# Performance work log

Measured on AMD Instinct MI355X. Metric: run time of the kernel, lower is better.

## Reference

```python
import jax, jax.numpy as jnp
import numpy as np

DIM, HEADS = 1536, 12
HD = DIM // HEADS            # 128 head dim
C = HD // 2                  # 64 complex (pair) dim
C0 = C - 2 * (C // 3)        # 22 (temporal axis)
C1 = C // 3                  # 21 (each spatial axis)
MAX_POS = 1024
F_, H_, W_ = 9, 22, 22
SEQ = F_ * H_ * W_           # 4356
NCLASS = 2
EPS = 1e-6


def _rope_tables():
    # Wan rope_params: theta = 10000, per-axis half-dims C0, C1, C1.
    def ang(half):
        inv = 1.0 / (10000.0 ** (np.arange(0, 2 * half, 2) / (2 * half)))
        return np.outer(np.arange(MAX_POS), inv)
    a = np.concatenate([ang(C0), ang(C1), ang(C1)], axis=1)  # [MAX_POS, C]
    return jnp.asarray(np.cos(a), jnp.float32), jnp.asarray(np.sin(a), jnp.float32)


def setup_inputs() -> dict:
    key = jax.random.key(0)
    ks = jax.random.split(key, 6)
    s = 1.0 / np.sqrt(DIM)
    def lin(k):
        k1, k2 = jax.random.split(k)
        return (jax.random.uniform(k1, (DIM, DIM), jnp.float32, -s, s),
                jax.random.uniform(k2, (DIM,), jnp.float32, -s, s))
    Wq, bq = lin(ks[0]); Wk, bk = lin(ks[1]); Wv, bv = lin(ks[2]); Wo, bo = lin(ks[3])
    fc, fs = _rope_tables()
    masks = (jax.random.uniform(ks[4], (NCLASS, H_ * W_)) < 0.5).astype(jnp.float32)
    x = jax.random.normal(ks[5], (1, SEQ, DIM), jnp.float32)
    return {"x": x, "Wq": Wq, "bq": bq, "Wk": Wk, "bk": bk, "Wv": Wv, "bv": bv,
            "Wo": Wo, "bo": bo, "gq": jnp.ones((DIM,), jnp.float32),
            "gk": jnp.ones((DIM,), jnp.float32), "freqs_cos": fc, "freqs_sin": fs,
            "ref_target_masks": masks, "f": F_, "h": H_, "w": W_}


def _rmsnorm(x, g):
    return x * jax.lax.rsqrt(jnp.mean(x * x, axis=-1, keepdims=True) + EPS) * g


def _grid_cs(tab, f, h, w):
    # per-position (f,h,w) rope table -> [f*h*w, C]
    p0 = jnp.broadcast_to(tab[:f, None, None, :C0], (f, h, w, C0))
    p1 = jnp.broadcast_to(tab[None, :h, None, C0:C0 + C1], (f, h, w, C1))
    p2 = jnp.broadcast_to(tab[None, None, :w, C0 + C1:], (f, h, w, C1))
    return jnp.concatenate([p0, p1, p2], axis=-1).reshape(f * h * w, C)


def _rope(x, cos, sin):
    # x: [b,s,n,d]; pairs are interleaved along d (view_as_complex semantics)
    b, s, n, d = x.shape
    xr = x.reshape(b, s, n, d // 2, 2)
    a, bi = xr[..., 0], xr[..., 1]
    cos = cos[None, :, None, :]
    sin = sin[None, :, None, :]
    out = jnp.stack([a * cos - bi * sin, a * sin + bi * cos], axis=-1)
    return out.reshape(b, s, n, d)


def reference(x, Wq, bq, Wk, bk, Wv, bv, Wo, bo, gq, gk, freqs_cos, freqs_sin,
              ref_target_masks, f, h, w):
    b, s, _ = x.shape
    n, d = HEADS, HD
    q = _rmsnorm(x @ Wq.T + bq, gq).reshape(b, s, n, d)
    k = _rmsnorm(x @ Wk.T + bk, gk).reshape(b, s, n, d)
    v = (x @ Wv.T + bv).reshape(b, s, n, d)
    cos = _grid_cs(freqs_cos, f, h, w)
    sin = _grid_cs(freqs_sin, f, h, w)
    q = _rope(q, cos, sin)
    k = _rope(k, cos, sin)
    scale = 1.0 / np.sqrt(d).astype(np.float32)
    # full (window_size == (-1,-1)) attention; seq_lens == s so k_lens mask is identity
    scores = jnp.einsum('bsnd,btnd->bnst', q, k) * scale
    p = jax.nn.softmax(scores, axis=-1)
    o = jnp.einsum('bnst,btnd->bsnd', p, v).reshape(b, s, n * d)
    out = o @ Wo.T + bo
    # aux attention map vs reference-frame keys (first h*w spatial tokens), no-grad path
    xs = h * w
    ref_k = k[:, :xs]
    s2 = jnp.einsum('bsnd,btnd->bnst', q * scale, ref_k)
    p2 = jax.nn.softmax(s2, axis=-1)                       # [b,n,s,xs]
    m = ref_target_masks                                   # [c,xs]
    maps = jnp.einsum('bnst,ct->cbns', p2, m) / jnp.sum(m, axis=-1)[:, None, None, None]
    attn_map = maps.mean(axis=2).reshape(-1, s)            # mean over heads -> [c*b, s]
    return out, attn_map
```

## Files before the change

kernel.cpp:

```cpp
#include <hip/hip_runtime.h>
#include <hip/hip_bf16.h>
#include <math.h>

constexpr int SEQ   = 4356;
constexpr int DIM   = 1536;
constexpr int HEADS = 12;
constexpr int HD    = 128;
constexpr int CH    = 64;
constexpr int C0c   = 22;
constexpr int C1c   = 21;
constexpr int WWc   = 22;
constexpr int HHWW  = 484;
constexpr int XS    = 484;
constexpr int KVB   = 32;
constexpr int NT    = (SEQ + KVB - 1) / KVB;
constexpr int SEQP  = 4416;
constexpr size_t SD = (size_t)SEQ * DIM;

typedef float f32x4 __attribute__((ext_vector_type(4)));
typedef short bf16x8 __attribute__((ext_vector_type(8)));
typedef short bf16x4 __attribute__((ext_vector_type(4)));

__device__ inline unsigned short f2bf(float f) {
  union { float f; unsigned u; } x; x.f = f;
  return (unsigned short)((x.u + 0x7FFFu + ((x.u >> 16) & 1u)) >> 16);
}

#define GLD16(g, l)                                                                        \
  __builtin_amdgcn_global_load_lds((const __attribute__((address_space(1))) unsigned*)    \
                                       (const void*)(g),                                  \
                                   (__attribute__((address_space(3))) unsigned*)(void*)(l),\
                                   16, 0, 0)

__global__ __launch_bounds__(256) void prep_kernel(const float* __restrict__ mask,
                                                   float* __restrict__ amap,
                                                   float* __restrict__ cnt,
                                                   float4* __restrict__ msk4) {
  int t = threadIdx.x;
  for (int i = t; i < 2 * SEQ; i += 256) amap[i] = 0.f;
  for (int i = t; i < 512; i += 256) {
    float4 v;
    v.x = (i < XS) ? mask[i] : 0.f;
    v.y = (i < XS) ? mask[XS + i] : 0.f;
    v.z = (i < XS) ? 1.f : 0.f;
    v.w = 0.f;
    msk4[i] = v;
  }
  float c0 = 0.f, c1 = 0.f;
  for (int i = t; i < XS; i += 256) { c0 += mask[i]; c1 += mask[XS + i]; }
  __shared__ float red0[256];
  __shared__ float red1[256];
  red0[t] = c0; red1[t] = c1;
  __syncthreads();
  for (int off = 128; off > 0; off >>= 1) {
    if (t < off) { red0[t] += red0[t + off]; red1[t] += red1[t + off]; }
    __syncthreads();
  }
  if (t == 0) { cnt[0] = red0[0]; cnt[1] = red1[0]; }
}

__global__ __launch_bounds__(256) void padzero(unsigned short* __restrict__ vt) {
  const int pad = SEQP - SEQ;
  const int total = DIM * pad;
  for (int i = blockIdx.x * 256 + threadIdx.x; i < total; i += gridDim.x * 256) {
    const int d = i / pad, c = i - d * pad;
    vt[(size_t)d * SEQP + SEQ + c] = 0;
  }
}

__global__ __launch_bounds__(256) void to_bf16(const float* __restrict__ in,
                                               unsigned short* __restrict__ out, int n4) {
  for (int i = blockIdx.x * 256 + threadIdx.x; i < n4; i += gridDim.x * 256) {
    const float4 v = ((const float4*)in)[i];
    ushort4 o;
    o.x = f2bf(v.x); o.y = f2bf(v.y); o.z = f2bf(v.z); o.w = f2bf(v.w);
    ((ushort4*)out)[i] = o;
  }
}

__global__ __launch_bounds__(256) void to_bf16_w(const float* __restrict__ W0, const float* __restrict__ W1,
                                                 const float* __restrict__ W2, const float* __restrict__ W3,
                                                 unsigned short* __restrict__ o0, unsigned short* __restrict__ o1,
                                                 unsigned short* __restrict__ o2, unsigned short* __restrict__ o3,
                                                 int n4) {
  const int z = blockIdx.z;
  const float* in = (z == 0) ? W0 : (z == 1) ? W1 : (z == 2) ? W2 : W3;
  unsigned short* out = (z == 0) ? o0 : (z == 1) ? o1 : (z == 2) ? o2 : o3;
  for (int i = blockIdx.x * 256 + threadIdx.x; i < n4; i += gridDim.x * 256) {
    const float4 v = ((const float4*)in)[i];
    ushort4 o;
    o.x = f2bf(v.x); o.y = f2bf(v.y); o.z = f2bf(v.z); o.w = f2bf(v.w);
    ((ushort4*)out)[i] = o;
  }
}

__global__ __launch_bounds__(256) void gemm_qkv(const unsigned short* __restrict__ A,
                                                const unsigned short* __restrict__ B0,
                                                const unsigned short* __restrict__ B1,
                                                const unsigned short* __restrict__ B2,
                                                const float* __restrict__ bq,
                                                const float* __restrict__ bk,
                                                const float* __restrict__ bv,
                                                float* __restrict__ o0,
                                                float* __restrict__ o1,
                                                unsigned short* __restrict__ vtout,
                                                int M) {
  __shared__ unsigned short As[128 * 64];
  __shared__ unsigned short Bs[128 * 64];
  const int z = blockIdx.z;
  const unsigned short* B = (z == 0) ? B0 : (z == 1) ? B1 : B2;
  const float* bias = (z == 0) ? bq : (z == 1) ? bk : bv;
  const int t    = threadIdx.x;
  const int lane = t & 63;
  const int w    = t >> 6;
  const int wr   = w >> 1, wc = w & 1;
  const int bm = blockIdx.x * 128, bn = blockIdx.y * 128;
  const int lq = lane & 15, lg = lane >> 4;
  f32x4 acc[4][4] = {};
  for (int k0 = 0; k0 < DIM; k0 += 64) {
#pragma unroll
    for (int i = 0; i < 4; ++i) {
      const int idx = i * 256 + t;
      const int row = idx >> 3;
      const int c8  = (idx & 7) * 8;
      const int ga  = min(bm + row, M - 1);
      GLD16(A + (size_t)ga * DIM + k0 + c8, As + idx * 8);
      const int gb  = bn + row;
      GLD16(B + (size_t)gb * DIM + k0 + c8, Bs + idx * 8);
    }
    __syncthreads();
#pragma unroll
    for (int kk = 0; kk < 2; ++kk) {
      bf16x8 af[4], bf[4];
#pragma unroll
      for (int m = 0; m < 4; ++m)
        af[m] = *(const bf16x8*)(As + (wr * 64 + m * 16 + lq) * 64 + kk * 32 + lg * 8);
#pragma unroll
      for (int n = 0; n < 4; ++n)
        bf[n] = *(const bf16x8*)(Bs + (wc * 64 + n * 16 + lq) * 64 + kk * 32 + lg * 8);
#pragma unroll
      for (int m = 0; m < 4; ++m)
#pragma unroll
        for (int n = 0; n < 4; ++n)
          acc[m][n] = __builtin_amdgcn_mfma_f32_16x16x32_bf16(af[m], bf[n], acc[m][n], 0, 0, 0);
    }
    __syncthreads();
  }
#pragma unroll
  for (int n = 0; n < 4; ++n) {
    const int col = bn + wc * 64 + n * 16 + lq;
    const float bv2 = bias[col];
#pragma unroll
    for (int m = 0; m < 4; ++m) {
      const int rm = bm + wr * 64 + m * 16 + lg * 4;
      if (z < 2) {
        float* C = (z == 0) ? o0 : o1;
#pragma unroll
        for (int r = 0; r < 4; ++r) {
          const int row = rm + r;
          if (row < M) C[(size_t)row * DIM + col] = acc[m][n][r] + bv2;
        }
      } else {
        if (rm < M) {
          bf16x4 o;
#pragma unroll
          for (int r = 0; r < 4; ++r) o[r] = (short)f2bf(acc[m][n][r] + bv2);
          *(bf16x4*)(vtout + (size_t)col * SEQP + rm) = o;
        }
      }
    }
  }
}

__global__ __launch_bounds__(256) void gemm_mfma(const unsigned short* __restrict__ A,
                                                 const unsigned short* __restrict__ B,
                                                 const float* __restrict__ bias,
                                                 float* __restrict__ C, int M) {
  __shared__ unsigned short As[128 * 64];
  __shared__ unsigned short Bs[128 * 64];
  const int t    = threadIdx.x;
  const int lane = t & 63;
  const int w    = t >> 6;
  const int wr   = w >> 1, wc = w & 1;
  const int bm = blockIdx.x * 128, bn = blockIdx.y * 128;
  const int lq = lane & 15, lg = lane >> 4;
  f32x4 acc[4][4] = {};
  for (int k0 = 0; k0 < DIM; k0 += 64) {
#pragma unroll
    for (int i = 0; i < 4; ++i) {
      const int idx = i * 256 + t;
      const int row = idx >> 3;
      const int c8  = (idx & 7) * 8;
      const int ga  = min(bm + row, M - 1);
      GLD16(A + (size_t)ga * DIM + k0 + c8, As + idx * 8);
      const int gb  = bn + row;
      GLD16(B + (size_t)gb * DIM + k0 + c8, Bs + idx * 8);
    }
    __syncthreads();
#pragma unroll
    for (int kk = 0; kk < 2; ++kk) {
      bf16x8 af[4], bf[4];
#pragma unroll
      for (int m = 0; m < 4; ++m)
        af[m] = *(const bf16x8*)(As + (wr * 64 + m * 16 + lq) * 64 + kk * 32 + lg * 8);
#pragma unroll
      for (int n = 0; n < 4; ++n)
        bf[n] = *(const bf16x8*)(Bs + (wc * 64 + n * 16 + lq) * 64 + kk * 32 + lg * 8);
#pragma unroll
      for (int m = 0; m < 4; ++m)
#pragma unroll
        for (int n = 0; n < 4; ++n)
          acc[m][n] = __builtin_amdgcn_mfma_f32_16x16x32_bf16(af[m], bf[n], acc[m][n], 0, 0, 0);
    }
    __syncthreads();
  }
#pragma unroll
  for (int n = 0; n < 4; ++n) {
    const int col = bn + wc * 64 + n * 16 + lq;
    const float bv = bias[col];
#pragma unroll
    for (int m = 0; m < 4; ++m) {
      const int rm = bm + wr * 64 + m * 16 + lg * 4;
#pragma unroll
      for (int r = 0; r < 4; ++r) {
        const int row = rm + r;
        if (row < M) C[(size_t)row * DIM + col] = acc[m][n][r] + bv;
      }
    }
  }
}

__global__ __launch_bounds__(256) void rms_rope2(const float* __restrict__ qy,
                                                 const float* __restrict__ ky,
                                                 const float* __restrict__ gq,
                                                 const float* __restrict__ gk,
                                                 const float* __restrict__ fcos,
                                                 const float* __restrict__ fsin,
                                                 unsigned short* __restrict__ qout,
                                                 unsigned short* __restrict__ kout) {
  const int z = blockIdx.y;
  const float* y = z ? ky : qy;
  const float* g = z ? gk : gq;
  unsigned short* outb = z ? kout : qout;
  const float scale = z ? 1.0f : 0.08838834764831845f;
  const int s = blockIdx.x;
  const float* row = y + (size_t)s * DIM;
  const int t = threadIdx.x;
  float ss = 0.f;
  for (int i = t; i < DIM / 4; i += 256) {
    const float4 v = ((const float4*)row)[i];
    ss += v.x * v.x + v.y * v.y + v.z * v.z + v.w * v.w;
  }
#pragma unroll
  for (int off = 1; off < 64; off <<= 1) ss += __shfl_xor(ss, off);
  __shared__ float wred[4];
  if ((t & 63) == 0) wred[t >> 6] = ss;
  __syncthreads();
  const float tot = wred[0] + wred[1] + wred[2] + wred[3];
  const float rs = rsqrtf(tot * (1.0f / DIM) + 1e-6f);
  const int fi  = s / HHWW;
  const int rem = s - fi * HHWW;
  const int hi  = rem / WWc;
  const int wi  = rem - hi * WWc;
  for (int p = t; p < DIM / 2; p += 256) {
    const int head = p >> 6;
    const int c    = p & 63;
    const int idx  = head * HD + 2 * c;
    const int trow = (c < C0c) ? fi : ((c < C0c + C1c) ? hi : wi);
    const float co = fcos[trow * CH + c];
    const float si = fsin[trow * CH + c];
    const float a  = row[idx] * rs * g[idx];
    const float b  = row[idx + 1] * rs * g[idx + 1];
    ushort2 pr;
    pr.x = f2bf((a * co - b * si) * scale);
    pr.y = f2bf((a * si + b * co) * scale);
    *(ushort2*)(outb + (size_t)s * DIM + idx) = pr;
  }
}

#define SOFT_QS(QS, SACC, MAP_, LAST_, KBV)                                                \
  {                                                                                        \
    float sv[8];                                                                           \
    _Pragma("unroll")                                                                      \
    for (int i = 0; i < 8; ++i) {                                                          \
      float v = SACC[i >> 2][i & 3];                                                       \
      if (LAST_) { const int key = (KBV) + (i >> 2) * 16 + lg * 4 + (i & 3);               \
                   if (key >= SEQ) v = -1e30f; }                                           \
      sv[i] = __expf(v);                                                                   \
      ls[QS] += sv[i];                                                                     \
    }                                                                                      \
    if (MAP_) {                                                                            \
      _Pragma("unroll")                                                                    \
      for (int i = 0; i < 8; ++i) {                                                        \
        const int key = (KBV) + (i >> 2) * 16 + lg * 4 + (i & 3);                          \
        const float4 mv = Msk[key];                                                        \
        n0[QS] = fmaf(sv[i], mv.x, n0[QS]);                                                \
        n1[QS] = fmaf(sv[i], mv.y, n1[QS]);                                                \
        d2[QS] = fmaf(sv[i], mv.z, d2[QS]);                                                \
      }                                                                                    \
    }                                                                                      \
    _Pragma("unroll")                                                                      \
    for (int kbi = 0; kbi < 2; ++kbi) {                                                    \
      unsigned r0, r1;                                                                     \
      asm("v_cvt_pk_bf16_f32 %0, %1, %2" : "=v"(r0) : "v"(sv[kbi*4+0]), "v"(sv[kbi*4+1])); \
      asm("v_cvt_pk_bf16_f32 %0, %1, %2" : "=v"(r1) : "v"(sv[kbi*4+2]), "v"(sv[kbi*4+3])); \
      uint2 pw; pw.x = r0; pw.y = r1;                                                      \
      *(uint2*)&Pw[QS][lq][kbi * 16 + lg * 4] = pw;                                        \
    }                                                                                      \
  }

#define TILE_BODY(KB_, MAP_, LAST_, PRE_)                                                  \
  {                                                                                        \
    const int kb_ = (KB_);                                                                 \
    const int cur_ = (kb_ >> 5) & 1;                                                       \
    const unsigned short* Kc = Ks[cur_];                                                   \
    const unsigned short* Vc = Vs[cur_];                                                   \
    if (PRE_) {                                                                            \
      unsigned short* Kn = Ks[cur_ ^ 1];                                                   \
      unsigned short* Vn = Vs[cur_ ^ 1];                                                   \
      const int kbn = kb_ + KVB;                                                           \
      _Pragma("unroll")                                                                    \
      for (int j = 0; j < 2; ++j) {                                                        \
        const int ck = t + j * 256;                                                        \
        const int kr = ck >> 4, ksl = ck & 15;                                             \
        GLD16(kh + (size_t)min(kbn + kr, SEQ - 1) * DIM + ((ksl ^ (kr & 7)) * 8),          \
              Kn + ck * 8);                                                                \
        const int vd = ck >> 2, vsl = ck & 3;                                              \
        GLD16(vh + (size_t)vd * SEQP + kbn + ((vsl ^ ((vd >> 1) & 3)) * 8),                \
              Vn + ck * 8);                                                                \
      }                                                                                    \
    }                                                                                      \
    f32x4 sacc0[2] = {}, sacc1[2] = {};                                                    \
    _Pragma("unroll")                                                                      \
    for (int kbi = 0; kbi < 2; ++kbi) {                                                    \
      const int krow = kbi * 16 + lq;                                                      \
      _Pragma("unroll")                                                                    \
      for (int c = 0; c < 4; ++c) {                                                        \
        const bf16x8 kf = *(const bf16x8*)(Kc + (krow * 16 + ((c * 4 + lg) ^ (krow & 7))) * 8); \
        sacc0[kbi] = __builtin_amdgcn_mfma_f32_16x16x32_bf16(kf, qf0[c], sacc0[kbi], 0, 0, 0);  \
        sacc1[kbi] = __builtin_amdgcn_mfma_f32_16x16x32_bf16(kf, qf1[c], sacc1[kbi], 0, 0, 0);  \
      }                                                                                    \
    }                                                                                      \
    SOFT_QS(0, sacc0, MAP_, LAST_, kb_)                                                    \
    SOFT_QS(1, sacc1, MAP_, LAST_, kb_)                                                    \
    {                                                                                      \
      const bf16x8 pf0 = *(const bf16x8*)&Pw[0][lq][lg * 8];                               \
      const bf16x8 pf1 = *(const bf16x8*)&Pw[1][lq][lg * 8];                               \
      _Pragma("unroll")                                                                    \
      for (int db = 0; db < 8; ++db) {                                                     \
        const int vd = db * 16 + lq;                                                       \
        const bf16x8 vf = *(const bf16x8*)(Vc + (vd * 4 + (lg ^ ((vd >> 1) & 3))) * 8);    \
        acc0[db] = __builtin_amdgcn_mfma_f32_16x16x32_bf16(vf, pf0, acc0[db], 0, 0, 0);    \
        acc1[db] = __builtin_amdgcn_mfma_f32_16x16x32_bf16(vf, pf1, acc1[db], 0, 0, 0);    \
      }                                                                                    \
    }                                                                                      \
    if (PRE_) __syncthreads();                                                             \
  }

__global__ __launch_bounds__(256, 3) void flash_mfma(const unsigned short* __restrict__ qbuf,
                                                     const unsigned short* __restrict__ kbuf,
                                                     const unsigned short* __restrict__ vt,
                                                     const float4* __restrict__ msk4,
                                                     const float* __restrict__ cnt,
                                                     unsigned short* __restrict__ ob,
                                                     float* __restrict__ amap) {
  const int h    = blockIdx.y;
  const int t    = threadIdx.x;
  const int w    = t >> 6;
  const int lane = t & 63;
  const int lq   = lane & 15, lg = lane >> 4;
  const int qbase = blockIdx.x * 128 + w * 32;

  __shared__ __align__(16) unsigned short Ks[2][KVB * 128];
  __shared__ __align__(16) unsigned short Vs[2][128 * KVB];
  __shared__ __align__(16) unsigned short Plds[4][2][16][40];
  __shared__ float4 Msk[512];
  unsigned short (*Pw)[16][40] = Plds[w];

  const unsigned short* kh = kbuf + h * HD;
  const unsigned short* vh = vt + (size_t)(h * HD) * SEQP;

  for (int i = t; i < 512; i += 256) Msk[i] = msk4[i];

  const int qsrc0 = min(qbase + lq, SEQ - 1);
  const int qsrc1 = min(qbase + 16 + lq, SEQ - 1);
  bf16x8 qf0[4], qf1[4];
#pragma unroll
  for (int c = 0; c < 4; ++c) {
    qf0[c] = *(const bf16x8*)(qbuf + (size_t)qsrc0 * DIM + h * HD + c * 32 + lg * 8);
    qf1[c] = *(const bf16x8*)(qbuf + (size_t)qsrc1 * DIM + h * HD + c * 32 + lg * 8);
  }

  f32x4 acc0[8] = {}, acc1[8] = {};
  float ls[2] = {0.f, 0.f};
  float d2[2] = {0.f, 0.f}, n0[2] = {0.f, 0.f}, n1[2] = {0.f, 0.f};

#pragma unroll
  for (int j = 0; j < 2; ++j) {
    const int ck = t + j * 256;
    const int kr = ck >> 4, ksl = ck & 15;
    GLD16(kh + (size_t)min(kr, SEQ - 1) * DIM + ((ksl ^ (kr & 7)) * 8), Ks[0] + ck * 8);
    const int vd = ck >> 2, vsl = ck & 3;
    GLD16(vh + (size_t)vd * SEQP + ((vsl ^ ((vd >> 1) & 3)) * 8), Vs[0] + ck * 8);
  }
  __syncthreads();

  for (int tile = 0; tile < 16; ++tile)         TILE_BODY(tile * KVB, true,  false, true);
  for (int tile = 16; tile < NT - 1; ++tile)    TILE_BODY(tile * KVB, false, false, true);
  TILE_BODY((NT - 1) * KVB, false, true, false);

#pragma unroll
  for (int qs = 0; qs < 2; ++qs) {
    ls[qs] += __shfl_xor(ls[qs], 16);
    ls[qs] += __shfl_xor(ls[qs], 32);
  }
  {
    const int qrow = qbase + lq;
    if (qrow < SEQ) {
      const float inv = 1.f / ls[0];
#pragma unroll
      for (int db = 0; db < 8; ++db) {
        bf16x4 o;
#pragma unroll
        for (int r = 0; r < 4; ++r) o[r] = (short)f2bf(acc0[db][r] * inv);
        *(bf16x4*)(ob + (size_t)qrow * DIM + h * HD + db * 16 + lg * 4) = o;
      }
    }
  }
  {
    const int qrow = qbase + 16 + lq;
    if (qrow < SEQ) {
      const float inv = 1.f / ls[1];
#pragma unroll
      for (int db = 0; db < 8; ++db) {
        bf16x4 o;
#pragma unroll
        for (int r = 0; r < 4; ++r) o[r] = (short)f2bf(acc1[db][r] * inv);
        *(bf16x4*)(ob + (size_t)qrow * DIM + h * HD + db * 16 + lg * 4) = o;
      }
    }
  }
#pragma unroll
  for (int qs = 0; qs < 2; ++qs) {
    float dd = d2[qs], a0 = n0[qs], a1 = n1[qs];
    dd += __shfl_xor(dd, 16); dd += __shfl_xor(dd, 32);
    a0 += __shfl_xor(a0, 16); a0 += __shfl_xor(a0, 32);
    a1 += __shfl_xor(a1, 16); a1 += __shfl_xor(a1, 32);
    const int qrow = qbase + qs * 16 + lq;
    if (lane < 16 && qrow < SEQ) {
      const float invd = 1.f / (dd * (float)HEADS);
      atomicAdd(&amap[qrow],       a0 * invd / cnt[0]);
      atomicAdd(&amap[SEQ + qrow], a1 * invd / cnt[1]);
    }
  }
}

extern "C" void kernel_launch(void* const* d_in, const int* in_sizes, int n_in,
                              void* d_out, int out_size, void* d_ws, size_t ws_size,
                              hipStream_t stream) {
  const float* x    = (const float*)d_in[0];
  const float* Wq   = (const float*)d_in[1];
  const float* bq   = (const float*)d_in[2];
  const float* Wk   = (const float*)d_in[3];
  const float* bk   = (const float*)d_in[4];
  const float* Wv   = (const float*)d_in[5];
  const float* bv   = (const float*)d_in[6];
  const float* Wo   = (const float*)d_in[7];
  const float* bo   = (const float*)d_in[8];
  const float* gq   = (const float*)d_in[9];
  const float* gk   = (const float*)d_in[10];
  const float* fc   = (const float*)d_in[11];
  const float* fs   = (const float*)d_in[12];
  const float* mask = (const float*)d_in[13];

  float* out  = (float*)d_out;
  float* amap = out + SD;
  float* f32a = out;

  float* f32b        = (float*)d_ws;
  unsigned short* xb = (unsigned short*)(f32b + SD);
  unsigned short* qb = xb + SD;
  unsigned short* kb = qb + SD;
  unsigned short* vt = kb + SD;
  unsigned short* wqb = vt + (size_t)DIM * SEQP;
  unsigned short* wkb = wqb + (size_t)DIM * DIM;
  unsigned short* wvb = wkb + (size_t)DIM * DIM;
  unsigned short* wob = wvb + (size_t)DIM * DIM;
  float4* msk4 = (float4*)(wob + (size_t)DIM * DIM);
  float* cnt  = (float*)(msk4 + 512);
  unsigned short* ob = (unsigned short*)f32b;

  prep_kernel<<<1, 256, 0, stream>>>(mask, amap, cnt, msk4);
  padzero<<<64, 256, 0, stream>>>(vt);
  to_bf16<<<2048, 256, 0, stream>>>(x, xb, (int)(SD / 4));
  constexpr int W4 = DIM * DIM / 4;
  to_bf16_w<<<dim3(512, 1, 4), 256, 0, stream>>>(Wq, Wk, Wv, Wo, wqb, wkb, wvb, wob, W4);

  const dim3 gg((SEQ + 127) / 128, DIM / 128, 3);
  gemm_qkv<<<gg, 256, 0, stream>>>(xb, wqb, wkb, wvb, bq, bk, bv, f32a, f32b, vt, SEQ);

  rms_rope2<<<dim3(SEQ, 2), 256, 0, stream>>>(f32a, f32b, gq, gk, fc, fs, qb, kb);

  const dim3 fg((SEQ + 127) / 128, HEADS);
  flash_mfma<<<fg, 256, 0, stream>>>(qb, kb, vt, msk4, cnt, ob, amap);

  const dim3 go((SEQ + 127) / 128, DIM / 128);
  gemm_mfma<<<go, 256, 0, stream>>>(ob, wob, bo, out, SEQ);
}
```

Baseline: 434.1 us.

## Split flash attention across two KV halves and merge with a combine kernel

Adds a second grid dimension so each query block's KV range is processed by two workgroups: the first takes tiles 0–63, including the reference-frame aux map, and the second takes the rest. Each writes unnormalised fp32 accumulators and row sums to scratch buffers. A new combine kernel adds the partials, normalises them and writes the bf16 attention output. The goal is to fill more CUs than the original 420-block grid. The cost is an extra launch plus a large fp32 partial write and read.

```diff
diff --git a/kernel.cpp b/kernel.cpp
--- a/kernel.cpp
+++ b/kernel.cpp
@@ -14,7 +14,9 @@
 constexpr int XS    = 484;
 constexpr int KVB   = 32;
 constexpr int NT    = (SEQ + KVB - 1) / KVB;
+constexpr int TSPLIT = 64;
 constexpr int SEQP  = 4416;
+constexpr int NHQ   = HEADS * SEQ;
 constexpr size_t SD = (size_t)SEQ * DIM;
 
 typedef float f32x4 __attribute__((ext_vector_type(4)));
@@ -362,9 +364,12 @@
                                                      const unsigned short* __restrict__ vt,
                                                      const float4* __restrict__ msk4,
                                                      const float* __restrict__ cnt,
-                                                     unsigned short* __restrict__ ob,
+                                                     float* __restrict__ pacc0,
+                                                     float* __restrict__ pacc1,
+                                                     float* __restrict__ pl,
                                                      float* __restrict__ amap) {
   const int h    = blockIdx.y;
+  const int z    = blockIdx.z;
   const int t    = threadIdx.x;
   const int w    = t >> 6;
   const int lane = t & 63;
@@ -395,63 +400,92 @@
   float ls[2] = {0.f, 0.f};
   float d2[2] = {0.f, 0.f}, n0[2] = {0.f, 0.f}, n1[2] = {0.f, 0.f};
 
+  const int tile0 = (z == 0) ? 0 : TSPLIT;
+  const int kb0   = tile0 * KVB;
+  unsigned short* K0 = Ks[tile0 & 1];
+  unsigned short* V0 = Vs[tile0 & 1];
 #pragma unroll
   for (int j = 0; j < 2; ++j) {
     const int ck = t + j * 256;
     const int kr = ck >> 4, ksl = ck & 15;
-    GLD16(kh + (size_t)min(kr, SEQ - 1) * DIM + ((ksl ^ (kr & 7)) * 8), Ks[0] + ck * 8);
+    GLD16(kh + (size_t)min(kb0 + kr, SEQ - 1) * DIM + ((ksl ^ (kr & 7)) * 8), K0 + ck * 8);
     const int vd = ck >> 2, vsl = ck & 3;
-    GLD16(vh + (size_t)vd * SEQP + ((vsl ^ ((vd >> 1) & 3)) * 8), Vs[0] + ck * 8);
+    GLD16(vh + (size_t)vd * SEQP + kb0 + ((vsl ^ ((vd >> 1) & 3)) * 8), V0 + ck * 8);
   }
   __syncthreads();
 
-  for (int tile = 0; tile < 16; ++tile)         TILE_BODY(tile * KVB, true,  false, true);
-  for (int tile = 16; tile < NT - 1; ++tile)    TILE_BODY(tile * KVB, false, false, true);
-  TILE_BODY((NT - 1) * KVB, false, true, false);
+  if (z == 0) {
+    for (int tile = 0; tile < 16; ++tile)           TILE_BODY(tile * KVB, true,  false, true);
+    for (int tile = 16; tile < TSPLIT - 1; ++tile)  TILE_BODY(tile * KVB, false, false, true);
+    TILE_BODY((TSPLIT - 1) * KVB, false, false, false);
+  } else {
+    for (int tile = TSPLIT; tile < NT - 1; ++tile)  TILE_BODY(tile * KVB, false, false, true);
+    TILE_BODY((NT - 1) * KVB, false, true, false);
+  }
 
 #pragma unroll
   for (int qs = 0; qs < 2; ++qs) {
     ls[qs] += __shfl_xor(ls[qs], 16);
     ls[qs] += __shfl_xor(ls[qs], 32);
   }
+  float* pz  = (z == 0) ? pacc0 : pacc1;
+  float* plz = pl + z * NHQ;
   {
     const int qrow = qbase + lq;
     if (qrow < SEQ) {
-      const float inv = 1.f / ls[0];
-#pragma unroll
-      for (int db = 0; db < 8; ++db) {
-        bf16x4 o;
-#pragma unroll
-        for (int r = 0; r < 4; ++r) o[r] = (short)f2bf(acc0[db][r] * inv);
-        *(bf16x4*)(ob + (size_t)qrow * DIM + h * HD + db * 16 + lg * 4) = o;
-      }
+      float* base = pz + ((size_t)(h * SEQ + qrow)) * HD;
+#pragma unroll
+      for (int db = 0; db < 8; ++db)
+        *(f32x4*)(base + db * 16 + lg * 4) = acc0[db];
+      if (lane < 16) plz[h * SEQ + qrow] = ls[0];
     }
   }
   {
     const int qrow = qbase + 16 + lq;
     if (qrow < SEQ) {
-      const float inv = 1.f / ls[1];
-#pragma unroll
-      for (int db = 0; db < 8; ++db) {
-        bf16x4 o;
-#pragma unroll
-        for (int r = 0; r < 4; ++r) o[r] = (short)f2bf(acc1[db][r] * inv);
-        *(bf16x4*)(ob + (size_t)qrow * DIM + h * HD + db * 16 + lg * 4) = o;
+      float* base = pz + ((size_t)(h * SEQ + qrow)) * HD;
+#pragma unroll
+      for (int db = 0; db < 8; ++db)
+        *(f32x4*)(base + db * 16 + lg * 4) = acc1[db];
+      if (lane < 16) plz[h * SEQ + qrow] = ls[1];
+    }
+  }
+  if (z == 0) {
+#pragma unroll
+    for (int qs = 0; qs < 2; ++qs) {
+      float dd = d2[qs], a0 = n0[qs], a1 = n1[qs];
+      dd += __shfl_xor(dd, 16); dd += __shfl_xor(dd, 32);
+      a0 += __shfl_xor(a0, 16); a0 += __shfl_xor(a0, 32);
+      a1 += __shfl_xor(a1, 16); a1 += __shfl_xor(a1, 32);
+      const int qrow = qbase + qs * 16 + lq;
+      if (lane < 16 && qrow < SEQ) {
+        const float invd = 1.f / (dd * (float)HEADS);
+        atomicAdd(&amap[qrow],       a0 * invd / cnt[0]);
+        atomicAdd(&amap[SEQ + qrow], a1 * invd / cnt[1]);
       }
     }
   }
-#pragma unroll
-  for (int qs = 0; qs < 2; ++qs) {
-    float dd = d2[qs], a0 = n0[qs], a1 = n1[qs];
-    dd += __shfl_xor(dd, 16); dd += __shfl_xor(dd, 32);
-    a0 += __shfl_xor(a0, 16); a0 += __shfl_xor(a0, 32);
-    a1 += __shfl_xor(a1, 16); a1 += __shfl_xor(a1, 32);
-    const int qrow = qbase + qs * 16 + lq;
-    if (lane < 16 && qrow < SEQ) {
-      const float invd = 1.f / (dd * (float)HEADS);
-      atomicAdd(&amap[qrow],       a0 * invd / cnt[0]);
-      atomicAdd(&amap[SEQ + qrow], a1 * invd / cnt[1]);
-    }
+}
+
+__global__ __launch_bounds__(256) void combine(const float* __restrict__ p0,
+                                               const float* __restrict__ p1,
+                                               const float* __restrict__ pl,
+                                               unsigned short* __restrict__ ob) {
+  const int n4 = (int)(SD / 4);
+  for (int i = blockIdx.x * 256 + threadIdx.x; i < n4; i += gridDim.x * 256) {
+    const int row = i >> 5;
+    const int d4  = (i & 31) << 2;
+    const float4 a = ((const float4*)p0)[i];
+    const float4 b = ((const float4*)p1)[i];
+    const float inv = 1.f / (pl[row] + pl[NHQ + row]);
+    const int hh = row / SEQ;
+    const int s  = row - hh * SEQ;
+    bf16x4 o;
+    o[0] = (short)f2bf((a.x + b.x) * inv);
+    o[1] = (short)f2bf((a.y + b.y) * inv);
+    o[2] = (short)f2bf((a.z + b.z) * inv);
+    o[3] = (short)f2bf((a.w + b.w) * inv);
+    *(bf16x4*)(ob + (size_t)s * DIM + hh * HD + d4) = o;
   }
 }
 
@@ -488,7 +522,8 @@
   unsigned short* wob = wvb + (size_t)DIM * DIM;
   float4* msk4 = (float4*)(wob + (size_t)DIM * DIM);
   float* cnt  = (float*)(msk4 + 512);
-  unsigned short* ob = (unsigned short*)f32b;
+  float* pl   = cnt + 8;
+  unsigned short* ob = xb;
 
   prep_kernel<<<1, 256, 0, stream>>>(mask, amap, cnt, msk4);
   padzero<<<64, 256, 0, stream>>>(vt);
@@ -501,8 +536,10 @@
 
   rms_rope2<<<dim3(SEQ, 2), 256, 0, stream>>>(f32a, f32b, gq, gk, fc, fs, qb, kb);
 
-  const dim3 fg((SEQ + 127) / 128, HEADS);
-  flash_mfma<<<fg, 256, 0, stream>>>(qb, kb, vt, msk4, cnt, ob, amap);
+  const dim3 fg((SEQ + 127) / 128, HEADS, 2);
+  flash_mfma<<<fg, 256, 0, stream>>>(qb, kb, vt, msk4, cnt, f32a, f32b, pl, amap);
+
+  combine<<<2048, 256, 0, stream>>>(f32a, f32b, pl, ob);
 
   const dim3 go((SEQ + 127) / 128, DIM / 128);
   gemm_mfma<<<go, 256, 0, stream>>>(ob, wob, bo, out, SEQ);
```

Result: slower. 462.2 us (+6.5%).
